# Performance work log

Measured on AMD Instinct MI355X. Metric: run time of the kernel, lower is better.

Reference implementation:

```python
import jax, jax.numpy as jnp
import numpy as np

B, L, D, H = 8, 2048, 1024, 1024
BASE_LR, BASE_WD = 0.01, 0.9


def setup_inputs() -> dict:
    key = jax.random.key(0)
    ks = jax.random.split(key, 8)
    s = 1.0 / np.sqrt(D)
    return {
        "x": jax.random.normal(ks[0], (B, L, D), jnp.float32),
        "hidden": jax.random.normal(ks[1], (B, D, H), jnp.float32),
        "log_base_lr": jnp.array([np.log(BASE_LR)], jnp.float32),
        "w_lr": jax.random.normal(ks[2], (D, 1), jnp.float32) * s,
        "b_lr": jnp.zeros((1,), jnp.float32),
        "log_base_wd": jnp.array([np.log(BASE_WD)], jnp.float32),
        "w_wd": jax.random.normal(ks[3], (D, 1), jnp.float32) * s,
        "b_wd": jnp.zeros((1,), jnp.float32),
        "w_q": jax.random.normal(ks[4], (D, H), jnp.float32) * s,
        "b_q": jnp.zeros((H,), jnp.float32),
        "w_k": jax.random.normal(ks[5], (D, H), jnp.float32) * s,
        "b_k": jnp.zeros((H,), jnp.float32),
        "w_v": jax.random.normal(ks[6], (D, D), jnp.float32) * s,
        "b_v": jnp.zeros((D,), jnp.float32),
    }


def reference(x, hidden, log_base_lr, w_lr, b_lr, log_base_wd, w_wd, b_wd,
              w_q, b_q, w_k, b_k, w_v, b_v):
    batch, length, dim = x.shape
    W_prev = hidden  # [b, d, h]
    query = x @ w_q + b_q                     # [b, l, h]
    key = x @ w_k + b_k                       # [b, l, h]
    value = x @ w_v + b_v                     # [b, l, d]
    lr = jnp.exp(log_base_lr) * jax.nn.sigmoid((x @ w_lr + b_lr)[..., 0])  # [b, l]
    # log(1 - base_wd * sigmoid(.)) via log1p for stability; same math.
    log_wd = jnp.log1p(-jnp.exp(log_base_wd) * jax.nn.sigmoid((x @ w_wd + b_wd)[..., 0]))  # [b, l]
    wd_cross = jnp.exp(jnp.cumsum(log_wd, axis=1))  # [b, l]
    # inner-chunk decay: entry [b, m, l] = exp(sum_{j=m+1..l} log_wd[b, j]) for l >= m
    tri = jnp.triu(jnp.broadcast_to(log_wd[:, None, :], (batch, length, length)), k=1)
    wd_inner = jnp.triu(jnp.exp(jnp.cumsum(tri, axis=2)))  # [b, l, l]
    kq = jnp.einsum('bld,bmd->blm', key, query)            # [b, l, m]
    mask_kq = kq * wd_inner
    WpK_V = jnp.einsum('bdh,blh->bld', W_prev, key) - value  # [b, l, d]
    y_inner = -jnp.einsum('bld,bl,blm->bmd', WpK_V, lr, mask_kq)
    y_cross = jnp.einsum('bdh,blh,bl->bld', W_prev, query, wd_cross)
    y = y_inner + y_cross
    W_next_inner = -jnp.einsum('bld,bl,blh->bdh', WpK_V, lr * wd_inner[:, :, -1], key)
    W_next_cross = W_prev * wd_cross[:, -1][:, None, None]
    W_next = W_next_inner + W_next_cross
    return y, W_next
```

## Files before the change

kernel.cpp:

```cpp
#include <hip/hip_runtime.h>
#include <stdint.h>

#define BB 8
#define LL 2048
#define DD 1024
#define HH 1024
#define BL (BB*LL)

typedef __attribute__((ext_vector_type(8))) short short8;
typedef __attribute__((ext_vector_type(4))) float f32x4;

__device__ __forceinline__ unsigned short f2bf(float f) {
  unsigned int x = __float_as_uint(f);
  unsigned int r = (x + 0x7fffu + ((x >> 16) & 1u)) >> 16;
  return (unsigned short)r;
}
__device__ __forceinline__ float bf2f(unsigned short u) {
  return __uint_as_float(((unsigned int)u) << 16);
}

#define TM 128
#define TN 128
#define BK 64

struct __align__(16) Smem {
  unsigned short a[TM*BK];
  unsigned short b[TN*BK];
};

__device__ __forceinline__ void stage16(const unsigned short* g, unsigned short* l) {
  __builtin_amdgcn_global_load_lds((const __attribute__((address_space(1))) void*)g,
                                   (__attribute__((address_space(3))) void*)l,
                                   16, 0, 0);
}

__device__ __forceinline__ void gemm_core(const unsigned short* __restrict__ A, int lda,
                                          const unsigned short* __restrict__ B, int ldb,
                                          int m0, int n0, int ktiles,
                                          Smem* sm, f32x4 acc[4][4]) {
  const int tid  = threadIdx.x;
  const int lane = tid & 63;
  const int wave = tid >> 6;
  const int mw = (wave >> 1) * 64;
  const int nw = (wave & 1) * 64;
  const int srow = lane >> 3;
  const int scol = (((lane & 7) ^ srow) * 8);
  const int fk = (lane >> 4) * 8;
  const int fr = lane & 15;
  const int fx = fr & 7;
  for (int kt = 0; kt < ktiles; ++kt) {
    const int k0 = kt * BK;
#pragma unroll
    for (int r = 0; r < 4; ++r) {
      const int chunk = wave * 4 + r;
      const int row = chunk * 8 + srow;
      stage16(A + (size_t)(m0 + row) * lda + (k0 + scol), &sm->a[chunk * 512]);
      stage16(B + (size_t)(n0 + row) * ldb + (k0 + scol), &sm->b[chunk * 512]);
    }
    __syncthreads();
#pragma unroll
    for (int kk = 0; kk < BK; kk += 32) {
      const int kc = ((((kk + fk) >> 3) ^ fx) << 3);
      short8 af[4], bfv[4];
#pragma unroll
      for (int i = 0; i < 4; ++i)
        af[i] = *(const short8*)&sm->a[(mw + i*16 + fr) * BK + kc];
#pragma unroll
      for (int j = 0; j < 4; ++j)
        bfv[j] = *(const short8*)&sm->b[(nw + j*16 + fr) * BK + kc];
#pragma unroll
      for (int i = 0; i < 4; ++i)
#pragma unroll
        for (int j = 0; j < 4; ++j)
          acc[i][j] = __builtin_amdgcn_mfma_f32_16x16x32_bf16(af[i], bfv[j], acc[i][j], 0, 0, 0);
    }
    __syncthreads();
  }
}

__device__ __forceinline__ void acc_init(f32x4 acc[4][4]) {
#pragma unroll
  for (int i = 0; i < 4; ++i)
#pragma unroll
    for (int j = 0; j < 4; ++j)
      acc[i][j] = (f32x4){0.f, 0.f, 0.f, 0.f};
}

template <typename F>
__device__ __forceinline__ void epilogue_loop(const f32x4 acc[4][4], F body) {
  const int lane_ = threadIdx.x & 63;
  const int wave_ = threadIdx.x >> 6;
  const int mw_ = (wave_ >> 1) * 64, nw_ = (wave_ & 1) * 64;
#pragma unroll
  for (int mi = 0; mi < 4; ++mi)
#pragma unroll
    for (int ni = 0; ni < 4; ++ni)
#pragma unroll
      for (int j = 0; j < 4; ++j) {
        const int rr = mw_ + mi * 16 + ((lane_ >> 4) << 2) + j;
        const int cc = nw_ + ni * 16 + (lane_ & 15);
        body(rr, cc, acc[mi][ni][j]);
      }
}


__global__ void k_prep_x(const float* __restrict__ x, const float* __restrict__ wlr,
                         const float* __restrict__ wwd, unsigned short* __restrict__ xb,
                         float* __restrict__ lrlog, float* __restrict__ wdlog) {
  const int wave = threadIdx.x >> 6, lane = threadIdx.x & 63;
  const int row = blockIdx.x * 4 + wave;
  const float* xr = x + (size_t)row * DD;
  float s1 = 0.f, s2 = 0.f;
#pragma unroll
  for (int ch = 0; ch < 4; ++ch) {
    const int col = ch * 256 + lane * 4;
    float4 v = *(const float4*)(xr + col);
    float4 a = *(const float4*)(wlr + col);
    float4 b = *(const float4*)(wwd + col);
    s1 += v.x*a.x + v.y*a.y + v.z*a.z + v.w*a.w;
    s2 += v.x*b.x + v.y*b.y + v.z*b.z + v.w*b.w;
    uint2 u;
    u.x = (unsigned)f2bf(v.x) | ((unsigned)f2bf(v.y) << 16);
    u.y = (unsigned)f2bf(v.z) | ((unsigned)f2bf(v.w) << 16);
    *(uint2*)(xb + (size_t)row * DD + col) = u;
  }
#pragma unroll
  for (int off = 32; off > 0; off >>= 1) {
    s1 += __shfl_down(s1, off);
    s2 += __shfl_down(s2, off);
  }
  if (lane == 0) { lrlog[row] = s1; wdlog[row] = s2; }
}

__global__ void k_prep_w(const float* __restrict__ wq, const float* __restrict__ wk,
                         const float* __restrict__ wv, unsigned short* __restrict__ wqt,
                         unsigned short* __restrict__ wkt, unsigned short* __restrict__ wvtn) {
  const int idx = blockIdx.x * 256 + threadIdx.x;
  const int k = idx >> 10, n = idx & 1023;
  const float* src = (blockIdx.z == 0) ? wq : (blockIdx.z == 1) ? wk : wv;
  unsigned short* dst = (blockIdx.z == 0) ? wqt : (blockIdx.z == 1) ? wkt : wvtn;
  float v = src[(size_t)k * 1024 + n];
  if (blockIdx.z == 2) v = -v;
  dst[(size_t)n * 1024 + k] = f2bf(v);
}

__global__ void k_prep_h(const float* __restrict__ hid, unsigned short* __restrict__ wpb) {
  const size_t i = ((size_t)blockIdx.x * 256 + threadIdx.x) * 4;
  float4 v = *(const float4*)(hid + i);
  uint2 u;
  u.x = (unsigned)f2bf(v.x) | ((unsigned)f2bf(v.y) << 16);
  u.y = (unsigned)f2bf(v.z) | ((unsigned)f2bf(v.w) << 16);
  *(uint2*)(wpb + i) = u;
}

__global__ void k_scan(const float* __restrict__ lrlog, const float* __restrict__ wdlog,
                       const float* __restrict__ lbl, const float* __restrict__ blr,
                       const float* __restrict__ lbw, const float* __restrict__ bwd,
                       float* __restrict__ lr, float* __restrict__ c,
                       float* __restrict__ s, float* __restrict__ ecl) {
  const int b = blockIdx.x, t = threadIdx.x;
  __shared__ float sums[256];
  const float elr = expf(lbl[0]);
  const float ewd = expf(lbw[0]);
  const float blr0 = blr[0], bwd0 = bwd[0];
  float lw[8];
  const float* wb = wdlog + (size_t)b * LL + t * 8;
  float tot = 0.f;
#pragma unroll
  for (int i = 0; i < 8; ++i) {
    float z = wb[i] + bwd0;
    float sig = 1.f / (1.f + expf(-z));
    tot += log1pf(-ewd * sig);
    lw[i] = tot;
  }
  sums[t] = tot;
  __syncthreads();
  for (int off = 1; off < 256; off <<= 1) {
    float v = (t >= off) ? sums[t - off] : 0.f;
    __syncthreads();
    sums[t] += v;
    __syncthreads();
  }
  const float prev = (t > 0) ? sums[t - 1] : 0.f;
  const float ctot = sums[255];
  const float* lb = lrlog + (size_t)b * LL + t * 8;
#pragma unroll
  for (int i = 0; i < 8; ++i) {
    const int idx = b * LL + t * 8 + i;
    const float ci = prev + lw[i];
    c[idx] = ci;
    float zl = lb[i] + blr0;
    float lri = elr / (1.f + expf(-zl));
    lr[idx] = lri;
    s[idx] = lri * expf(ctot - ci);
  }
  if (t == 0) ecl[b] = expf(ctot);
}


__global__ __launch_bounds__(256) void k_gemm_q(const unsigned short* __restrict__ xb,
    const unsigned short* __restrict__ wt, const float* __restrict__ bias,
    const float* __restrict__ c, unsigned short* __restrict__ outb,
    unsigned short* __restrict__ q2b) {
  __shared__ Smem sm;
  f32x4 acc[4][4]; acc_init(acc);
  const int m0 = blockIdx.y * TM, n0 = blockIdx.x * TN;
  gemm_core(xb, DD, wt, DD, m0, n0, DD / BK, &sm, acc);
  epilogue_loop(acc, [&](int rr, int cc, float av) {
    const int row = m0 + rr, col = n0 + cc;
    const float v = av + bias[col];
    outb[(size_t)row * HH + col] = f2bf(v);
    q2b[(size_t)row * HH + col] = f2bf(v * __expf(c[row]));
  });
}

__global__ __launch_bounds__(256) void k_gemm_k(const unsigned short* __restrict__ xb,
    const unsigned short* __restrict__ wt, const float* __restrict__ bias,
    const float* __restrict__ s, unsigned short* __restrict__ kb,
    unsigned short* __restrict__ k2t) {
  __shared__ Smem sm;
  f32x4 acc[4][4]; acc_init(acc);
  const int m0 = blockIdx.y * TM, n0 = blockIdx.x * TN;
  gemm_core(xb, DD, wt, DD, m0, n0, DD / BK, &sm, acc);
  const int lane = threadIdx.x & 63, wave = threadIdx.x >> 6;
  const int mw = (wave >> 1) * 64, nw = (wave & 1) * 64;
#pragma unroll
  for (int mi = 0; mi < 4; ++mi)
#pragma unroll
    for (int ni = 0; ni < 4; ++ni) {
      const int col = n0 + nw + ni*16 + (lane & 15);
      const float bias_c = bias[col];
      const int row0 = m0 + mw + mi*16 + ((lane >> 4) << 2);
      const int b = row0 >> 11, ml0 = row0 & 2047;
      unsigned short tmp[4];
#pragma unroll
      for (int j = 0; j < 4; ++j) {
        float v = acc[mi][ni][j] + bias_c;
        kb[(size_t)(row0 + j) * HH + col] = f2bf(v);
        tmp[j] = f2bf(v * s[row0 + j]);
      }
      uint2 u;
      u.x = (unsigned)tmp[0] | ((unsigned)tmp[1] << 16);
      u.y = (unsigned)tmp[2] | ((unsigned)tmp[3] << 16);
      *(uint2*)&k2t[((size_t)b * HH + col) * LL + ml0] = u;
    }
}

__global__ __launch_bounds__(256) void k_gemm_u(const unsigned short* __restrict__ kb,
    const unsigned short* __restrict__ wpb, const unsigned short* __restrict__ xb,
    const unsigned short* __restrict__ wvtn, const float* __restrict__ bv,
    unsigned short* __restrict__ ut) {
  __shared__ Smem sm;
  f32x4 acc[4][4]; acc_init(acc);
  const int m0 = blockIdx.y * TM, n0 = blockIdx.x * TN;
  const int b = m0 >> 11;
  gemm_core(kb, HH, wpb + (size_t)b * DD * HH, HH, m0, n0, HH / BK, &sm, acc);
  gemm_core(xb, DD, wvtn, DD, m0, n0, DD / BK, &sm, acc);
  const int lane = threadIdx.x & 63, wave = threadIdx.x >> 6;
  const int mw = (wave >> 1) * 64, nw = (wave & 1) * 64;
#pragma unroll
  for (int mi = 0; mi < 4; ++mi)
#pragma unroll
    for (int ni = 0; ni < 4; ++ni) {
      const int col = n0 + nw + ni*16 + (lane & 15);
      const float bvc = bv[col];
      const int row0 = m0 + mw + mi*16 + ((lane >> 4) << 2);
      const int ml0 = row0 & 2047;
      unsigned short tmp[4];
#pragma unroll
      for (int j = 0; j < 4; ++j) tmp[j] = f2bf(acc[mi][ni][j] - bvc);
      uint2 u;
      u.x = (unsigned)tmp[0] | ((unsigned)tmp[1] << 16);
      u.y = (unsigned)tmp[2] | ((unsigned)tmp[3] << 16);
      *(uint2*)&ut[((size_t)b * DD + col) * LL + ml0] = u;
    }
}

__global__ __launch_bounds__(256) void k_gemm_p(const unsigned short* __restrict__ qb,
    const unsigned short* __restrict__ kb, const float* __restrict__ lr,
    const float* __restrict__ c, unsigned short* __restrict__ pb) {
  const int b = blockIdx.z;
  const int i = blockIdx.x;
  const int t = (i & 7) * 17 + (i >> 3);
  int mt = (int)((sqrtf(8.0f * (float)t + 1.0f) - 1.0f) * 0.5f);
  while ((mt + 1) * (mt + 2) / 2 <= t) ++mt;
  while (mt * (mt + 1) / 2 > t) --mt;
  const int nt = t - mt * (mt + 1) / 2;
  __shared__ Smem sm;
  f32x4 acc[4][4]; acc_init(acc);
  const int base = b * LL;
  const int m0g = base + mt * TM, n0g = base + nt * TN;
  gemm_core(qb, HH, kb, HH, m0g, n0g, HH / BK, &sm, acc);

  const int lane = threadIdx.x & 63, wave = threadIdx.x >> 6;
  const int mw = (wave >> 1) * 64, nw = (wave & 1) * 64;
  if (nt != mt) {
    const float cref = c[base + mt * TM];
    float er[4][4], fc[4];
#pragma unroll
    for (int mi = 0; mi < 4; ++mi)
#pragma unroll
      for (int j = 0; j < 4; ++j) {
        const int m = mt * TM + mw + mi*16 + ((lane >> 4) << 2) + j;
        er[mi][j] = __expf(c[base + m] - cref);
      }
#pragma unroll
    for (int ni = 0; ni < 4; ++ni) {
      const int l = nt * TN + nw + ni*16 + (lane & 15);
      fc[ni] = lr[base + l] * __expf(cref - c[base + l]);
    }
#pragma unroll
    for (int mi = 0; mi < 4; ++mi)
#pragma unroll
      for (int ni = 0; ni < 4; ++ni) {
        const int l = nt * TN + nw + ni*16 + (lane & 15);
        const int row0 = mt * TM + mw + mi*16 + ((lane >> 4) << 2);
#pragma unroll
        for (int j = 0; j < 4; ++j) {
          const float v = -acc[mi][ni][j] * er[mi][j] * fc[ni];
          pb[((size_t)base + row0 + j) * LL + l] = f2bf(v);
        }
      }
  } else {
    epilogue_loop(acc, [&](int rr, int cc, float av) {
      const int m = mt * TM + rr, l = nt * TN + cc;
      float v = 0.f;
      if (l <= m) v = -av * lr[base + l] * __expf(c[base + m] - c[base + l]);
      pb[((size_t)base + m) * LL + l] = f2bf(v);
    });
  }
}

__global__ __launch_bounds__(256) void k_gemm_y(const unsigned short* __restrict__ pb,
    const unsigned short* __restrict__ ut, const unsigned short* __restrict__ q2b,
    const unsigned short* __restrict__ wpb, float* __restrict__ out) {
  const int b = blockIdx.z, mt = blockIdx.y, nt = blockIdx.x;
  __shared__ Smem sm;
  f32x4 acc[4][4]; acc_init(acc);
  gemm_core(pb + (size_t)b * LL * LL, LL, ut + (size_t)b * DD * LL, LL,
            mt * TM, nt * TN, (mt + 1) * 2, &sm, acc);
  gemm_core(q2b, HH, wpb + (size_t)b * DD * HH, HH,
            b * LL + mt * TM, nt * TN, HH / BK, &sm, acc);
  epilogue_loop(acc, [&](int rr, int cc, float av) {
    const int m = mt * TM + rr, d = nt * TN + cc;
    out[((size_t)b * LL + m) * DD + d] = av;
  });
}

__global__ __launch_bounds__(256) void k_gemm_wn(const unsigned short* __restrict__ ut,
    const unsigned short* __restrict__ k2t, const float* __restrict__ hid,
    const float* __restrict__ ecl, float* __restrict__ out2) {
  const int b = blockIdx.z, mt = blockIdx.y, nt = blockIdx.x;
  __shared__ Smem sm;
  f32x4 acc[4][4]; acc_init(acc);
  gemm_core(ut + (size_t)b * DD * LL, LL, k2t + (size_t)b * HH * LL, LL,
            mt * TM, nt * TN, LL / BK, &sm, acc);
  epilogue_loop(acc, [&](int rr, int cc, float av) {
    const int d = mt * TM + rr, h = nt * TN + cc;
    const size_t gi = ((size_t)b * DD + d) * HH + h;
    out2[gi] = -av + ecl[b] * hid[gi];
  });
}


extern "C" void kernel_launch(void* const* d_in, const int* in_sizes, int n_in,
                              void* d_out, int out_size, void* d_ws, size_t ws_size,
                              hipStream_t stream) {
  (void)in_sizes; (void)n_in; (void)out_size; (void)ws_size;
  const float* x   = (const float*)d_in[0];
  const float* hid = (const float*)d_in[1];
  const float* lbl = (const float*)d_in[2];
  const float* wlr = (const float*)d_in[3];
  const float* blr = (const float*)d_in[4];
  const float* lbw = (const float*)d_in[5];
  const float* wwd = (const float*)d_in[6];
  const float* bwd = (const float*)d_in[7];
  const float* wq  = (const float*)d_in[8];
  const float* bq  = (const float*)d_in[9];
  const float* wk  = (const float*)d_in[10];
  const float* bk  = (const float*)d_in[11];
  const float* wv  = (const float*)d_in[12];
  const float* bv  = (const float*)d_in[13];
  float* out = (float*)d_out;

  char* w = (char*)d_ws;
  constexpr size_t SZ_XB  = (size_t)BL * DD * 2;
  constexpr size_t SZ_QB  = (size_t)BL * HH * 2;
  constexpr size_t SZ_KB  = (size_t)BL * HH * 2;
  constexpr size_t SZ_K2T = (size_t)BB * HH * LL * 2;
  constexpr size_t SZ_UT  = (size_t)BB * DD * LL * 2;
  constexpr size_t SZ_PB  = (size_t)BB * LL * LL * 2;
  constexpr size_t SZ_WT  = (size_t)DD * HH * 2;
  constexpr size_t SZ_WPB = (size_t)BB * DD * HH * 2;
  constexpr size_t SZ_V16 = (size_t)BL * 4;

  size_t off = 0;
  unsigned short* xb   = (unsigned short*)(w + off); off += SZ_XB;
  unsigned short* qb   = (unsigned short*)(w + off); off += SZ_QB;
  unsigned short* kb   = (unsigned short*)(w + off); off += SZ_KB;
  unsigned short* k2t  = (unsigned short*)(w + off); off += SZ_K2T;
  unsigned short* ut   = (unsigned short*)(w + off); off += SZ_UT;
  unsigned short* pb   = (unsigned short*)(w + off); off += SZ_PB;
  unsigned short* wqt  = (unsigned short*)(w + off); off += SZ_WT;
  unsigned short* wkt  = (unsigned short*)(w + off); off += SZ_WT;
  unsigned short* wvtn = (unsigned short*)(w + off); off += SZ_WT;
  unsigned short* wpb  = (unsigned short*)(w + off); off += SZ_WPB;
  float* lrlog = (float*)(w + off); off += SZ_V16;
  float* wdlog = (float*)(w + off); off += SZ_V16;
  float* lr    = (float*)(w + off); off += SZ_V16;
  float* c     = (float*)(w + off); off += SZ_V16;
  float* s     = (float*)(w + off); off += SZ_V16;
  float* ecl   = (float*)(w + off); off += 256;

  unsigned short* q2b = (unsigned short*)(out + (size_t)BL * DD);
  float* out2 = out + (size_t)BL * DD;

  k_prep_x<<<dim3(BL / 4), 256, 0, stream>>>(x, wlr, wwd, xb, lrlog, wdlog);
  k_prep_w<<<dim3(4096, 1, 3), 256, 0, stream>>>(wq, wk, wv, wqt, wkt, wvtn);
  k_prep_h<<<dim3((unsigned)((size_t)BB * DD * HH / 1024)), 256, 0, stream>>>(hid, wpb);
  k_scan<<<dim3(BB), 256, 0, stream>>>(lrlog, wdlog, lbl, blr, lbw, bwd, lr, c, s, ecl);

  k_gemm_q<<<dim3(HH / TN, BL / TM), 256, 0, stream>>>(xb, wqt, bq, c, qb, q2b);
  k_gemm_k<<<dim3(HH / TN, BL / TM), 256, 0, stream>>>(xb, wkt, bk, s, kb, k2t);
  k_gemm_u<<<dim3(DD / TN, BL / TM), 256, 0, stream>>>(kb, wpb, xb, wvtn, bv, ut);
  k_gemm_p<<<dim3(136, 1, BB), 256, 0, stream>>>(qb, kb, lr, c, pb);
  k_gemm_y<<<dim3(DD / TN, LL / TM, BB), 256, 0, stream>>>(pb, ut, q2b, wpb, out);
  k_gemm_wn<<<dim3(HH / TN, DD / TM, BB), 256, 0, stream>>>(ut, k2t, hid, ecl, out2);
}
```

Measured before the change: 699.0 us.

## Fold W_prev·W_k into per-batch combined weight and remap tiles for XCD locality

The U = W_prev·K − V computation changes from two chained GEMMs over K and X into a single GEMM of X against a precomputed per-batch matrix W_prev·W_kᵀ − W_v, with the bias folded into a per-row bias2 vector. This removes the dependency of k_gemm_u on k_gemm_k and cuts one 1024-deep K-loop per tile. In exchange it adds a small batched 1024×1024 GEMM and a bias reduction, and rounds the combined weight to bf16. Block indices for the q/k/u/y/wn GEMMs are also remapped so tiles sharing operands land on the same XCD for L2 reuse, and y interleaves its triangular M tiles for load balance.

```diff
diff --git a/kernel.cpp b/kernel.cpp
--- a/kernel.cpp
+++ b/kernel.cpp
@@ -103,6 +103,14 @@
       }
 }
 
+__device__ __forceinline__ void xcd_map_u(int x, int i, int& bb, int& mt, int& nt) {
+  bb = i >> 4;
+  const int i16 = i & 15;
+  const int sr = x >> 1, sc = x & 1;
+  mt = 4 * (i16 & 3) + sr;
+  nt = 4 * sc + (i16 >> 2);
+}
+
 
 __global__ void k_prep_x(const float* __restrict__ x, const float* __restrict__ wlr,
                          const float* __restrict__ wwd, unsigned short* __restrict__ xb,
@@ -134,8 +142,10 @@
 
 __global__ void k_prep_w(const float* __restrict__ wq, const float* __restrict__ wk,
                          const float* __restrict__ wv, unsigned short* __restrict__ wqt,
-                         unsigned short* __restrict__ wkt, unsigned short* __restrict__ wvtn) {
+                         unsigned short* __restrict__ wkt, unsigned short* __restrict__ wvtn,
+                         unsigned short* __restrict__ wkr) {
   const int idx = blockIdx.x * 256 + threadIdx.x;
+  if (blockIdx.z == 3) { wkr[idx] = f2bf(wk[idx]); return; }
   const int k = idx >> 10, n = idx & 1023;
   const float* src = (blockIdx.z == 0) ? wq : (blockIdx.z == 1) ? wk : wv;
   unsigned short* dst = (blockIdx.z == 0) ? wqt : (blockIdx.z == 1) ? wkt : wvtn;
@@ -151,6 +161,24 @@
   u.x = (unsigned)f2bf(v.x) | ((unsigned)f2bf(v.y) << 16);
   u.y = (unsigned)f2bf(v.z) | ((unsigned)f2bf(v.w) << 16);
   *(uint2*)(wpb + i) = u;
+}
+
+__global__ void k_bias2(const unsigned short* __restrict__ wpb, const float* __restrict__ bk,
+                        const float* __restrict__ bv, float* __restrict__ bias2) {
+  const int wave = threadIdx.x >> 6, lane = threadIdx.x & 63;
+  const int row = blockIdx.x * 4 + wave;
+  const unsigned short* wr = wpb + (size_t)row * HH;
+  float s = 0.f;
+#pragma unroll
+  for (int ch = 0; ch < 4; ++ch) {
+    const int col = ch * 256 + lane * 4;
+    float4 a = *(const float4*)(bk + col);
+    ushort4 u = *(const ushort4*)(wr + col);
+    s += a.x * bf2f(u.x) + a.y * bf2f(u.y) + a.z * bf2f(u.z) + a.w * bf2f(u.w);
+  }
+#pragma unroll
+  for (int off = 32; off > 0; off >>= 1) s += __shfl_down(s, off);
+  if (lane == 0) bias2[row] = s - bv[row & 1023];
 }
 
 __global__ void k_scan(const float* __restrict__ lrlog, const float* __restrict__ wdlog,
@@ -198,13 +226,28 @@
 }
 
 
+__global__ __launch_bounds__(256) void k_gemm_m2(const unsigned short* __restrict__ wpb,
+    const unsigned short* __restrict__ wkr, const unsigned short* __restrict__ wvtn,
+    unsigned short* __restrict__ w2t) {
+  const int b = blockIdx.z, mt = blockIdx.y, nt = blockIdx.x;
+  __shared__ Smem sm;
+  f32x4 acc[4][4]; acc_init(acc);
+  gemm_core(wpb + (size_t)b * DD * HH, HH, wkr, HH, mt * TM, nt * TN, HH / BK, &sm, acc);
+  epilogue_loop(acc, [&](int rr, int cc, float av) {
+    const int d = mt * TM + rr, j = nt * TN + cc;
+    const size_t gi = (size_t)d * DD + j;
+    w2t[(size_t)b * DD * DD + gi] = f2bf(av + bf2f(wvtn[gi]));
+  });
+}
+
 __global__ __launch_bounds__(256) void k_gemm_q(const unsigned short* __restrict__ xb,
     const unsigned short* __restrict__ wt, const float* __restrict__ bias,
     const float* __restrict__ c, unsigned short* __restrict__ outb,
     unsigned short* __restrict__ q2b) {
-  __shared__ Smem sm;
-  f32x4 acc[4][4]; acc_init(acc);
-  const int m0 = blockIdx.y * TM, n0 = blockIdx.x * TN;
+  int bb, mt, nt; xcd_map_u(blockIdx.x, blockIdx.y, bb, mt, nt);
+  const int m0 = (bb * 16 + mt) * TM, n0 = nt * TN;
+  __shared__ Smem sm;
+  f32x4 acc[4][4]; acc_init(acc);
   gemm_core(xb, DD, wt, DD, m0, n0, DD / BK, &sm, acc);
   epilogue_loop(acc, [&](int rr, int cc, float av) {
     const int row = m0 + rr, col = n0 + cc;
@@ -218,9 +261,10 @@
     const unsigned short* __restrict__ wt, const float* __restrict__ bias,
     const float* __restrict__ s, unsigned short* __restrict__ kb,
     unsigned short* __restrict__ k2t) {
-  __shared__ Smem sm;
-  f32x4 acc[4][4]; acc_init(acc);
-  const int m0 = blockIdx.y * TM, n0 = blockIdx.x * TN;
+  int bb, mt, nt; xcd_map_u(blockIdx.x, blockIdx.y, bb, mt, nt);
+  const int m0 = (bb * 16 + mt) * TM, n0 = nt * TN;
+  __shared__ Smem sm;
+  f32x4 acc[4][4]; acc_init(acc);
   gemm_core(xb, DD, wt, DD, m0, n0, DD / BK, &sm, acc);
   const int lane = threadIdx.x & 63, wave = threadIdx.x >> 6;
   const int mw = (wave >> 1) * 64, nw = (wave & 1) * 64;
@@ -246,16 +290,15 @@
     }
 }
 
-__global__ __launch_bounds__(256) void k_gemm_u(const unsigned short* __restrict__ kb,
-    const unsigned short* __restrict__ wpb, const unsigned short* __restrict__ xb,
-    const unsigned short* __restrict__ wvtn, const float* __restrict__ bv,
+__global__ __launch_bounds__(256) void k_gemm_u(const unsigned short* __restrict__ xb,
+    const unsigned short* __restrict__ w2t, const float* __restrict__ bias2,
     unsigned short* __restrict__ ut) {
-  __shared__ Smem sm;
-  f32x4 acc[4][4]; acc_init(acc);
-  const int m0 = blockIdx.y * TM, n0 = blockIdx.x * TN;
-  const int b = m0 >> 11;
-  gemm_core(kb, HH, wpb + (size_t)b * DD * HH, HH, m0, n0, HH / BK, &sm, acc);
-  gemm_core(xb, DD, wvtn, DD, m0, n0, DD / BK, &sm, acc);
+  int bb, mt, nt; xcd_map_u(blockIdx.x, blockIdx.y, bb, mt, nt);
+  const int m0 = (bb * 16 + mt) * TM, n0 = nt * TN;
+  const int b = bb;
+  __shared__ Smem sm;
+  f32x4 acc[4][4]; acc_init(acc);
+  gemm_core(xb, DD, w2t + (size_t)b * DD * DD, DD, m0, n0, DD / BK, &sm, acc);
   const int lane = threadIdx.x & 63, wave = threadIdx.x >> 6;
   const int mw = (wave >> 1) * 64, nw = (wave & 1) * 64;
 #pragma unroll
@@ -263,12 +306,12 @@
 #pragma unroll
     for (int ni = 0; ni < 4; ++ni) {
       const int col = n0 + nw + ni*16 + (lane & 15);
-      const float bvc = bv[col];
+      const float b2c = bias2[b * DD + col];
       const int row0 = m0 + mw + mi*16 + ((lane >> 4) << 2);
       const int ml0 = row0 & 2047;
       unsigned short tmp[4];
 #pragma unroll
-      for (int j = 0; j < 4; ++j) tmp[j] = f2bf(acc[mi][ni][j] - bvc);
+      for (int j = 0; j < 4; ++j) tmp[j] = f2bf(acc[mi][ni][j] + b2c);
       uint2 u;
       u.x = (unsigned)tmp[0] | ((unsigned)tmp[1] << 16);
       u.y = (unsigned)tmp[2] | ((unsigned)tmp[3] << 16);
@@ -334,7 +377,13 @@
 __global__ __launch_bounds__(256) void k_gemm_y(const unsigned short* __restrict__ pb,
     const unsigned short* __restrict__ ut, const unsigned short* __restrict__ q2b,
     const unsigned short* __restrict__ wpb, float* __restrict__ out) {
-  const int b = blockIdx.z, mt = blockIdx.y, nt = blockIdx.x;
+  const int b = blockIdx.z;
+  const int x = blockIdx.x, i16 = blockIdx.y;
+  const int sr = x >> 1, sc = x & 1;
+  const int lm = i16 & 3, ln = i16 >> 2;
+  const int mt = (lm == 0) ? (15 - sr) : (lm == 1) ? (8 + sr)
+               : (lm == 2) ? (7 - sr)  : sr;
+  const int nt = 4 * sc + ln;
   __shared__ Smem sm;
   f32x4 acc[4][4]; acc_init(acc);
   gemm_core(pb + (size_t)b * LL * LL, LL, ut + (size_t)b * DD * LL, LL,
@@ -350,7 +399,11 @@
 __global__ __launch_bounds__(256) void k_gemm_wn(const unsigned short* __restrict__ ut,
     const unsigned short* __restrict__ k2t, const float* __restrict__ hid,
     const float* __restrict__ ecl, float* __restrict__ out2) {
-  const int b = blockIdx.z, mt = blockIdx.y, nt = blockIdx.x;
+  const int b = blockIdx.z;
+  const int x = blockIdx.x, i8 = blockIdx.y;
+  const int sr = x >> 2, sc = x & 3;
+  const int mt = 4 * sr + (i8 & 3);
+  const int nt = 2 * sc + (i8 >> 2);
   __shared__ Smem sm;
   f32x4 acc[4][4]; acc_init(acc);
   gemm_core(ut + (size_t)b * DD * LL, LL, k2t + (size_t)b * HH * LL, LL,
@@ -411,19 +464,25 @@
   float* c     = (float*)(w + off); off += SZ_V16;
   float* s     = (float*)(w + off); off += SZ_V16;
   float* ecl   = (float*)(w + off); off += 256;
+  float* bias2 = (float*)(w + off); off += (size_t)BB * DD * 4;
+
+  unsigned short* w2t = pb;
+  unsigned short* wkr = pb + (size_t)BB * DD * DD;
 
   unsigned short* q2b = (unsigned short*)(out + (size_t)BL * DD);
   float* out2 = out + (size_t)BL * DD;
 
   k_prep_x<<<dim3(BL / 4), 256, 0, stream>>>(x, wlr, wwd, xb, lrlog, wdlog);
-  k_prep_w<<<dim3(4096, 1, 3), 256, 0, stream>>>(wq, wk, wv, wqt, wkt, wvtn);
+  k_prep_w<<<dim3(4096, 1, 4), 256, 0, stream>>>(wq, wk, wv, wqt, wkt, wvtn, wkr);
   k_prep_h<<<dim3((unsigned)((size_t)BB * DD * HH / 1024)), 256, 0, stream>>>(hid, wpb);
   k_scan<<<dim3(BB), 256, 0, stream>>>(lrlog, wdlog, lbl, blr, lbw, bwd, lr, c, s, ecl);
-
-  k_gemm_q<<<dim3(HH / TN, BL / TM), 256, 0, stream>>>(xb, wqt, bq, c, qb, q2b);
-  k_gemm_k<<<dim3(HH / TN, BL / TM), 256, 0, stream>>>(xb, wkt, bk, s, kb, k2t);
-  k_gemm_u<<<dim3(DD / TN, BL / TM), 256, 0, stream>>>(kb, wpb, xb, wvtn, bv, ut);
+  k_bias2<<<dim3(BB * DD / 4), 256, 0, stream>>>(wpb, bk, bv, bias2);
+
+  k_gemm_m2<<<dim3(DD / TN, DD / TM, BB), 256, 0, stream>>>(wpb, wkr, wvtn, w2t);
+  k_gemm_q<<<dim3(8, BL / TM / 16 * 16), 256, 0, stream>>>(xb, wqt, bq, c, qb, q2b);
+  k_gemm_k<<<dim3(8, BL / TM), 256, 0, stream>>>(xb, wkt, bk, s, kb, k2t);
+  k_gemm_u<<<dim3(8, BL / TM), 256, 0, stream>>>(xb, w2t, bias2, ut);
   k_gemm_p<<<dim3(136, 1, BB), 256, 0, stream>>>(qb, kb, lr, c, pb);
-  k_gemm_y<<<dim3(DD / TN, LL / TM, BB), 256, 0, stream>>>(pb, ut, q2b, wpb, out);
-  k_gemm_wn<<<dim3(HH / TN, DD / TM, BB), 256, 0, stream>>>(ut, k2t, hid, ecl, out2);
-}
+  k_gemm_y<<<dim3(8, 16, BB), 256, 0, stream>>>(pb, ut, q2b, wpb, out);
+  k_gemm_wn<<<dim3(8, 8, BB), 256, 0, stream>>>(ut, k2t, hid, ecl, out2);
+}
```

Measured after the change: 665.5 us. 1.05x faster.
